# Performance work log

Measured on AMD Instinct MI355X. Metric: run time of the kernel, lower is better.

Reference implementation:

```python
import jax, jax.numpy as jnp
import numpy as np

N_ATOMS = 8000
N_PAIRS = 80000
NF_IN = 32
NF_OUT = 32
N_DIST = 16
N_COMP = 4      # l_max=1: [l=0 (1), l=1 (3)] tensor components
N_INV = 2       # _invariant_counts[(2, 1)]
MIND_SOFT = 0.85
MAXD_SOFT = 5.0
HARD_CUTOFF = 6.5
GN_EPS = 1e-5


def _sensitivity(dist, mu, sigma):
    # HIP-NN style inverse-distance Gaussians with smooth cos^2 cutoff.
    inv_d = 1.0 / dist                                   # (P,)
    base = jnp.exp(-0.5 * ((inv_d[:, None] - mu) / sigma) ** 2)  # (P, n_dist)
    cut = jnp.where(dist < HARD_CUTOFF,
                    jnp.cos(0.5 * jnp.pi * dist / HARD_CUTOFF) ** 2, 0.0)
    return base * cut[:, None]


def setup_inputs() -> dict:
    key = jax.random.key(0)
    ks = jax.random.split(key, 10)
    in_features = jax.random.normal(ks[0], (N_ATOMS, NF_IN), jnp.float32)
    pair_first = jnp.sort(jax.random.randint(ks[1], (N_PAIRS,), 0, N_ATOMS))
    pair_second = jax.random.randint(ks[2], (N_PAIRS,), 0, N_ATOMS)
    dist_pairs = (0.5 + (HARD_CUTOFF - 0.5)
                  * jax.random.uniform(ks[3], (N_PAIRS,), jnp.float32))
    tensor_rhats = jax.random.normal(ks[4], (N_PAIRS, N_COMP), jnp.float32)
    # learned params
    sens_mu = jnp.linspace(1.0 / MAXD_SOFT, 1.0 / MIND_SOFT, N_DIST).astype(jnp.float32)
    sens_sigma = jnp.full((N_DIST,), float(sens_mu[1] - sens_mu[0]), jnp.float32)
    s_int = (2.0 / (N_DIST * NF_IN + NF_OUT)) ** 0.5
    int_weights = s_int * jax.random.normal(ks[5], (N_DIST, NF_OUT, NF_IN), jnp.float32)
    s_self = (2.0 / (NF_IN + NF_OUT)) ** 0.5
    selfint_w = s_self * jax.random.normal(ks[6], (NF_OUT, NF_IN), jnp.float32)
    selfint_b = jnp.zeros((NF_OUT,), jnp.float32)
    s_mix = (2.0 / (N_INV * NF_OUT + NF_OUT)) ** 0.5
    mixing_weights = s_mix * jax.random.normal(ks[7], (NF_OUT, N_INV, NF_OUT), jnp.float32)
    gn_weight = jnp.ones((N_INV * NF_OUT,), jnp.float32)
    gn_bias = jnp.zeros((N_INV * NF_OUT,), jnp.float32)
    return {
        "in_features": in_features, "tensor_rhats": tensor_rhats,
        "dist_pairs": dist_pairs, "int_weights": int_weights,
        "selfint_w": selfint_w, "selfint_b": selfint_b,
        "mixing_weights": mixing_weights, "gn_weight": gn_weight,
        "gn_bias": gn_bias, "sens_mu": sens_mu, "sens_sigma": sens_sigma,
        "pair_first": pair_first, "pair_second": pair_second,
    }


def reference(in_features, tensor_rhats, dist_pairs, int_weights,
              selfint_w, selfint_b, mixing_weights, gn_weight, gn_bias,
              sens_mu, sens_sigma, pair_first, pair_second):
    n_atoms = in_features.shape[0]
    # self interaction (Linear)
    self_part = in_features @ selfint_w.T + selfint_b          # (N, nf_out)
    # tensor sensitivities: (P, n_comp, n_dist) -> flat (P, n_comp*n_dist)
    sense = _sensitivity(dist_pairs, sens_mu, sens_sigma)      # (P, n_dist)
    sense_flat = (tensor_rhats[:, :, None] * sense[:, None, :]).reshape(
        -1, N_COMP * N_DIST)
    # envsum: env[a, s, f] = sum_{p: pair_first[p]=a} sense_flat[p, s] * feat[pair_second[p], f]
    feat_j = in_features[pair_second]                          # (P, nf_in)
    contrib = sense_flat[:, :, None] * feat_j[:, None, :]      # (P, S, nf_in)
    env = jax.ops.segment_sum(contrib, pair_first, num_segments=n_atoms)
    # interaction weights contraction
    w_rs = jnp.transpose(int_weights, (0, 2, 1)).reshape(N_DIST * NF_IN, NF_OUT)
    env_rs = env.reshape(n_atoms * N_COMP, N_DIST * NF_IN)
    tf = (env_rs @ w_rs).reshape(n_atoms, N_COMP, NF_OUT)
    tf = jnp.transpose(tf, (0, 2, 1))                          # (N, nf_out, n_comp)
    # HopInvariantLayer (n_max=2, l_max=1): [l=0 scalar, |l=1 vector|^2]
    invariants = jnp.stack(
        [tf[..., 0], jnp.sum(tf[..., 1:] ** 2, axis=-1)], axis=-1)  # (N, nf_out, 2)
    # GroupNorm over channels (n_inv groups of nf_out channels)
    x = jnp.transpose(invariants, (0, 2, 1))                   # (N, n_inv, nf_out)
    mean = jnp.mean(x, axis=-1, keepdims=True)
    var = jnp.var(x, axis=-1, keepdims=True)
    xn = (x - mean) / jnp.sqrt(var + GN_EPS)
    xn = xn * gn_weight.reshape(N_INV, NF_OUT) + gn_bias.reshape(N_INV, NF_OUT)
    norm_inv = jnp.transpose(xn, (0, 2, 1)).reshape(n_atoms, NF_OUT * N_INV)
    mix = norm_inv @ mixing_weights.reshape(NF_OUT * N_INV, NF_OUT)
    return mix + self_part
```

## Files before the change

kernel.cpp:

```cpp
#include <hip/hip_runtime.h>
#include <hip/hip_bf16.h>
#include <stdint.h>

#define GN_EPS 1e-5f

typedef __fp16 half2_t __attribute__((ext_vector_type(2)));
typedef __fp16 v8h __attribute__((ext_vector_type(8)));
typedef float v4f __attribute__((ext_vector_type(4)));
union U32H2 { uint32_t u; half2_t h; };
union U4V8 { uint4 u; v8h h; };
union UF { uint32_t u; float f; };

__device__ __forceinline__ float ldin(const void* p, int i, bool bf) {
    if (bf) {
        UF c; c.u = ((uint32_t)((const uint16_t*)p)[i]) << 16;
        return c.f;
    }
    return ((const float*)p)[i];
}

__device__ __forceinline__ uint16_t f2bf(float x) {
    union { float f; uint32_t u; } c; c.f = x;
    uint32_t u = c.u;
    return (uint16_t)((u + 0x7FFFu + ((u >> 16) & 1u)) >> 16);
}

__device__ __forceinline__ bool detect_bf16(const void* gnw) {
    uint32_t det = *(const uint32_t*)gnw;
    return (det >> 16) == (det & 0xFFFFu);
}

__device__ __forceinline__ uint32_t pkh2(float lo, float hi) {
    U32H2 u; u.h = __builtin_amdgcn_cvt_pkrtz(lo, hi); return u.u;
}

__global__ __launch_bounds__(256) void k0_prep(
    const void* __restrict__ feat, const void* __restrict__ rhats,
    const void* __restrict__ dists, const void* __restrict__ intw,
    const void* __restrict__ selfw, const void* __restrict__ selfb,
    const void* __restrict__ mw, const void* __restrict__ gnw,
    const void* __restrict__ gnb, const void* __restrict__ mu,
    const void* __restrict__ sig, const int* __restrict__ pf,
    int* __restrict__ seg, uint32_t* __restrict__ Wmf,
    float* __restrict__ featf, float4* __restrict__ rc4,
    float2* __restrict__ dj2, const int* __restrict__ ps,
    float* __restrict__ mwf, uint32_t* __restrict__ selfh,
    float* __restrict__ gnwf, float* __restrict__ gnbf,
    float* __restrict__ selfbf, float* __restrict__ muf,
    float* __restrict__ isgf, int n_atoms, int n_pairs)
{
    const bool bf = detect_bf16(gnw);
    const int tid = blockIdx.x * 256 + threadIdx.x;

    if (tid < n_pairs) {
        int a0 = pf[tid];
        if (tid == 0) { for (int a = 0; a <= a0; ++a) seg[a] = 0; }
        if (tid + 1 < n_pairs) {
            int a1 = pf[tid + 1];
            for (int a = a0 + 1; a <= a1; ++a) seg[a] = tid + 1;
        } else {
            for (int a = a0 + 1; a <= n_atoms; ++a) seg[a] = n_pairs;
        }
        float dist = ldin(dists, tid, bf);
        float cd = __cosf(0.2416609733530613f * dist);
        float cut = (dist < 6.5f) ? cd * cd : 0.0f;
        float4 rc;
        rc.x = ldin(rhats, 4 * tid + 0, bf) * cut;
        rc.y = ldin(rhats, 4 * tid + 1, bf) * cut;
        rc.z = ldin(rhats, 4 * tid + 2, bf) * cut;
        rc.w = ldin(rhats, 4 * tid + 3, bf) * cut;
        rc4[tid] = rc;
        float2 dj; dj.x = 1.0f / dist; dj.y = __int_as_float(ps[tid]);
        dj2[tid] = dj;
    }
    {
        int i0 = tid * 4;
#pragma unroll
        for (int k = 0; k < 4; ++k) {
            int i = i0 + k;
            if (i < n_atoms * 32) featf[i] = ldin(feat, i, bf);
        }
    }
    if (tid < 8192) {
        int fp = tid & 15, d = (tid >> 4) & 15, o = tid >> 8;
        float wlo = ldin(intw, (d * 32 + o) * 32 + 2 * fp, bf);
        float whi = ldin(intw, (d * 32 + o) * 32 + 2 * fp + 1, bf);
        Wmf[tid] = pkh2(wlo, whi);
    }
    if (tid < 2048) mwf[tid] = ldin(mw, tid, bf);
    if (tid < 512) {
        int fp = tid & 15, o = tid >> 4;
        selfh[tid] = pkh2(ldin(selfw, o * 32 + 2 * fp, bf),
                          ldin(selfw, o * 32 + 2 * fp + 1, bf));
    }
    if (tid < 64) { gnwf[tid] = ldin(gnw, tid, bf); gnbf[tid] = ldin(gnb, tid, bf); }
    if (tid < 32) selfbf[tid] = ldin(selfb, tid, bf);
    if (tid < 16) { muf[tid] = ldin(mu, tid, bf); isgf[tid] = 1.0f / ldin(sig, tid, bf); }
}

__global__ __launch_bounds__(256, 4) void k2_main(
    const int* __restrict__ seg, const uint32_t* __restrict__ Wmf,
    const float* __restrict__ featf, const float4* __restrict__ rc4,
    const float2* __restrict__ dj2, const float* __restrict__ mwf,
    const uint32_t* __restrict__ selfh, const float* __restrict__ gnwf,
    const float* __restrict__ gnbf, const float* __restrict__ selfbf,
    const float* __restrict__ muf, const float* __restrict__ isgf,
    const void* __restrict__ gnw, void* __restrict__ out, int n_atoms)
{
    __shared__ uint32_t envs[16 * 256];
    __shared__ float tfs[4 * 32 * 4];
    __shared__ float selfs[4][32];
    __shared__ float mwTs[32 * 68];
    __shared__ float xns[4][64];

    const int t = threadIdx.x, wv = t >> 6, lane = t & 63;
    const int a0 = blockIdx.x * 4;
    int a = a0 + wv;
    const bool astore = (a < n_atoms);
    if (!astore) a = n_atoms - 1;

    {
        int o = t & 31, kc = t >> 5;
#pragma unroll
        for (int i = 0; i < 8; ++i) {
            int k = kc * 8 + i;
            mwTs[o * 68 + k] = mwf[k * 32 + o];
        }
    }

    const int dD = lane >> 2, fq = lane & 3;
    const float mu_d = muf[dD], isg_d = isgf[dD];

    float env[4][8];
#pragma unroll
    for (int c = 0; c < 4; ++c)
#pragma unroll
        for (int fl = 0; fl < 8; ++fl) env[c][fl] = 0.0f;

    const int s = seg[a], e = seg[a + 1];

    for (int p = s; p < e; p += 4) {
        float2 dj[4]; float4 rc[4];
#pragma unroll
        for (int i = 0; i < 4; ++i) {
            int pi = (p + i < e) ? p + i : e - 1;
            dj[i] = dj2[pi];
            float4 r = rc4[pi];
            if (p + i >= e) r = make_float4(0.f, 0.f, 0.f, 0.f);
            rc[i] = r;
        }
        float4 fa[4], fb[4];
#pragma unroll
        for (int i = 0; i < 4; ++i) {
            const float4* fr = (const float4*)(featf +
                (size_t)__float_as_int(dj[i].y) * 32) + fq * 2;
            fa[i] = fr[0]; fb[i] = fr[1];
        }
#pragma unroll
        for (int i = 0; i < 4; ++i) {
            float x = (dj[i].x - mu_d) * isg_d;
            float sd = __expf(-0.5f * x * x);
            float t0 = sd * rc[i].x, t1 = sd * rc[i].y;
            float t2 = sd * rc[i].z, t3 = sd * rc[i].w;
            float fj[8] = {fa[i].x, fa[i].y, fa[i].z, fa[i].w,
                           fb[i].x, fb[i].y, fb[i].z, fb[i].w};
#pragma unroll
            for (int fl = 0; fl < 8; ++fl) {
                env[0][fl] = fmaf(t0, fj[fl], env[0][fl]);
                env[1][fl] = fmaf(t1, fj[fl], env[1][fl]);
                env[2][fl] = fmaf(t2, fj[fl], env[2][fl]);
                env[3][fl] = fmaf(t3, fj[fl], env[3][fl]);
            }
        }
    }

    {
        const int ci = dD * 4 + fq;
#pragma unroll
        for (int c = 0; c < 4; ++c) {
            int m = wv * 4 + c;
            uint4 w;
            w.x = pkh2(env[c][0], env[c][1]);
            w.y = pkh2(env[c][2], env[c][3]);
            w.z = pkh2(env[c][4], env[c][5]);
            w.w = pkh2(env[c][6], env[c][7]);
            *(uint4*)&envs[m * 256 + ((ci ^ m) << 2)] = w;
        }
    }
    __syncthreads();

    const int mrow = lane & 15, quad = lane >> 4;
    const int tile = wv >> 1;
    const int og = tile * 16 + mrow;
    if ((wv & 1) == 0) {
        v4f acc = {0.f, 0.f, 0.f, 0.f};
        const uint4* wb = (const uint4*)Wmf + (og * 64 + quad);
#pragma unroll
        for (int kk = 0; kk < 16; ++kk) {
            int cia = kk * 4 + quad;
            U4V8 Af, Bf;
            Af.u = *(const uint4*)&envs[mrow * 256 + ((cia ^ mrow) << 2)];
            Bf.u = wb[kk * 4];
            acc = __builtin_amdgcn_mfma_f32_16x16x32_f16(Af.h, Bf.h, acc, 0, 0, 0);
        }
        float4 st; st.x = acc[0]; st.y = acc[1]; st.z = acc[2]; st.w = acc[3];
        *(float4*)&tfs[(quad * 32 + og) * 4] = st;
    } else {
        int ar = a0 + (mrow < 4 ? mrow : 0);
        if (ar >= n_atoms) ar = n_atoms - 1;
        const float4* fp4 = (const float4*)(featf + (size_t)ar * 32 + quad * 8);
        float4 x = fp4[0], y = fp4[1];
        U4V8 Af, Bf;
        Af.u = make_uint4(pkh2(x.x, x.y), pkh2(x.z, x.w),
                          pkh2(y.x, y.y), pkh2(y.z, y.w));
        Bf.u = *(const uint4*)(selfh + og * 16 + quad * 4);
        v4f acc = {0.f, 0.f, 0.f, 0.f};
        acc = __builtin_amdgcn_mfma_f32_16x16x32_f16(Af.h, Bf.h, acc, 0, 0, 0);
        if (quad == 0) {
#pragma unroll
            for (int r = 0; r < 4; ++r)
                selfs[r][og] = acc[r];
        }
    }
    __syncthreads();

    const int o = lane & 31, half = lane >> 5;
    float4 tf = *(const float4*)&tfs[(wv * 32 + o) * 4];
    float inv0 = tf.x;
    float inv1 = tf.y * tf.y + tf.z * tf.z + tf.w * tf.w;

    float s0 = inv0, q0 = inv0 * inv0, s1 = inv1, q1 = inv1 * inv1;
#pragma unroll
    for (int m = 16; m >= 1; m >>= 1) {
        s0 += __shfl_xor(s0, m, 32);
        q0 += __shfl_xor(q0, m, 32);
        s1 += __shfl_xor(s1, m, 32);
        q1 += __shfl_xor(q1, m, 32);
    }
    float mean0 = s0 * (1.f / 32.f), mean1 = s1 * (1.f / 32.f);
    float var0 = q0 * (1.f / 32.f) - mean0 * mean0;
    float var1 = q1 * (1.f / 32.f) - mean1 * mean1;
    float xn0 = (inv0 - mean0) * rsqrtf(var0 + GN_EPS);
    float xn1 = (inv1 - mean1) * rsqrtf(var1 + GN_EPS);
    xn0 = xn0 * gnwf[o] + gnbf[o];
    xn1 = xn1 * gnwf[32 + o] + gnbf[32 + o];

    if (half == 0) *(float2*)&xns[wv][2 * o] = make_float2(xn0, xn1);

    float mix = 0.0f;
#pragma unroll
    for (int c = 0; c < 16; ++c) {
        float4 xk = *(const float4*)&xns[wv][c * 4];
        float4 w4 = *(const float4*)&mwTs[o * 68 + c * 4];
        mix = fmaf(xk.x, w4.x, mix);
        mix = fmaf(xk.y, w4.y, mix);
        mix = fmaf(xk.z, w4.z, mix);
        mix = fmaf(xk.w, w4.w, mix);
    }

    float res = mix + selfs[wv][o] + selfbf[o];
    if (half == 0 && astore) {
        if (detect_bf16(gnw)) ((uint16_t*)out)[a * 32 + o] = f2bf(res);
        else                  ((float*)out)[a * 32 + o]    = res;
    }
}

extern "C" void kernel_launch(void* const* d_in, const int* in_sizes, int n_in,
                              void* d_out, int out_size, void* d_ws, size_t ws_size,
                              hipStream_t stream) {
    const void* feat  = d_in[0];
    const void* rhats = d_in[1];
    const void* dists = d_in[2];
    const void* intw  = d_in[3];
    const void* selfw = d_in[4];
    const void* selfb = d_in[5];
    const void* mw    = d_in[6];
    const void* gnw   = d_in[7];
    const void* gnb   = d_in[8];
    const void* mu    = d_in[9];
    const void* sig   = d_in[10];
    const int* pf     = (const int*)d_in[11];
    const int* ps     = (const int*)d_in[12];

    const int n_pairs = in_sizes[11];
    const int n_atoms = in_sizes[0] / 32;

    char* ws = (char*)d_ws;
    int*      seg    = (int*)(ws + 0);
    uint32_t* Wmf    = (uint32_t*)(ws + 32768);
    float*    featf  = (float*)(ws + 65536);
    float4*   rc4    = (float4*)(ws + 1089536);
    float2*   dj2    = (float2*)(ws + 2369536);
    float*    mwf    = (float*)(ws + 3009536);
    uint32_t* selfh  = (uint32_t*)(ws + 3017728);
    float*    gnwf   = (float*)(ws + 3021824);
    float*    gnbf   = (float*)(ws + 3022080);
    float*    selfbf = (float*)(ws + 3022336);
    float*    muf    = (float*)(ws + 3022464);
    float*    isgf   = (float*)(ws + 3022528);

    int thr = n_pairs;
    int feat_thr = (n_atoms * 32 + 3) / 4;
    if (feat_thr > thr) thr = feat_thr;
    if (thr < 8192) thr = 8192;
    hipLaunchKernelGGL(k0_prep, dim3((thr + 255) / 256), dim3(256), 0, stream,
                       feat, rhats, dists, intw, selfw, selfb, mw, gnw, gnb,
                       mu, sig, pf, seg, Wmf, featf, rc4, dj2, ps, mwf,
                       selfh, gnwf, gnbf, selfbf, muf, isgf, n_atoms, n_pairs);
    hipLaunchKernelGGL(k2_main, dim3((n_atoms + 3) / 4), dim3(256), 0, stream,
                       seg, Wmf, featf, rc4, dj2, mwf, selfh, gnwf, gnbf,
                       selfbf, muf, isgf, gnw, d_out, n_atoms);
}
```

Before: 110.4 us.

## Fuse prep kernel into main kernel and binary-search pair segments per atom

```diff
diff --git a/kernel.cpp b/kernel.cpp
--- a/kernel.cpp
+++ b/kernel.cpp
@@ -19,6 +19,9 @@
     return ((const float*)p)[i];
 }
 
+__device__ __forceinline__ float bfl(uint32_t u) { UF c; c.u = u << 16; return c.f; }
+__device__ __forceinline__ float bfh(uint32_t u) { UF c; c.u = u & 0xFFFF0000u; return c.f; }
+
 __device__ __forceinline__ uint16_t f2bf(float x) {
     union { float f; uint32_t u; } c; c.f = x;
     uint32_t u = c.u;
@@ -34,78 +37,15 @@
     U32H2 u; u.h = __builtin_amdgcn_cvt_pkrtz(lo, hi); return u.u;
 }
 
-__global__ __launch_bounds__(256) void k0_prep(
+__global__ __launch_bounds__(256, 4) void k_fused(
     const void* __restrict__ feat, const void* __restrict__ rhats,
     const void* __restrict__ dists, const void* __restrict__ intw,
     const void* __restrict__ selfw, const void* __restrict__ selfb,
     const void* __restrict__ mw, const void* __restrict__ gnw,
     const void* __restrict__ gnb, const void* __restrict__ mu,
     const void* __restrict__ sig, const int* __restrict__ pf,
-    int* __restrict__ seg, uint32_t* __restrict__ Wmf,
-    float* __restrict__ featf, float4* __restrict__ rc4,
-    float2* __restrict__ dj2, const int* __restrict__ ps,
-    float* __restrict__ mwf, uint32_t* __restrict__ selfh,
-    float* __restrict__ gnwf, float* __restrict__ gnbf,
-    float* __restrict__ selfbf, float* __restrict__ muf,
-    float* __restrict__ isgf, int n_atoms, int n_pairs)
-{
-    const bool bf = detect_bf16(gnw);
-    const int tid = blockIdx.x * 256 + threadIdx.x;
-
-    if (tid < n_pairs) {
-        int a0 = pf[tid];
-        if (tid == 0) { for (int a = 0; a <= a0; ++a) seg[a] = 0; }
-        if (tid + 1 < n_pairs) {
-            int a1 = pf[tid + 1];
-            for (int a = a0 + 1; a <= a1; ++a) seg[a] = tid + 1;
-        } else {
-            for (int a = a0 + 1; a <= n_atoms; ++a) seg[a] = n_pairs;
-        }
-        float dist = ldin(dists, tid, bf);
-        float cd = __cosf(0.2416609733530613f * dist);
-        float cut = (dist < 6.5f) ? cd * cd : 0.0f;
-        float4 rc;
-        rc.x = ldin(rhats, 4 * tid + 0, bf) * cut;
-        rc.y = ldin(rhats, 4 * tid + 1, bf) * cut;
-        rc.z = ldin(rhats, 4 * tid + 2, bf) * cut;
-        rc.w = ldin(rhats, 4 * tid + 3, bf) * cut;
-        rc4[tid] = rc;
-        float2 dj; dj.x = 1.0f / dist; dj.y = __int_as_float(ps[tid]);
-        dj2[tid] = dj;
-    }
-    {
-        int i0 = tid * 4;
-#pragma unroll
-        for (int k = 0; k < 4; ++k) {
-            int i = i0 + k;
-            if (i < n_atoms * 32) featf[i] = ldin(feat, i, bf);
-        }
-    }
-    if (tid < 8192) {
-        int fp = tid & 15, d = (tid >> 4) & 15, o = tid >> 8;
-        float wlo = ldin(intw, (d * 32 + o) * 32 + 2 * fp, bf);
-        float whi = ldin(intw, (d * 32 + o) * 32 + 2 * fp + 1, bf);
-        Wmf[tid] = pkh2(wlo, whi);
-    }
-    if (tid < 2048) mwf[tid] = ldin(mw, tid, bf);
-    if (tid < 512) {
-        int fp = tid & 15, o = tid >> 4;
-        selfh[tid] = pkh2(ldin(selfw, o * 32 + 2 * fp, bf),
-                          ldin(selfw, o * 32 + 2 * fp + 1, bf));
-    }
-    if (tid < 64) { gnwf[tid] = ldin(gnw, tid, bf); gnbf[tid] = ldin(gnb, tid, bf); }
-    if (tid < 32) selfbf[tid] = ldin(selfb, tid, bf);
-    if (tid < 16) { muf[tid] = ldin(mu, tid, bf); isgf[tid] = 1.0f / ldin(sig, tid, bf); }
-}
-
-__global__ __launch_bounds__(256, 4) void k2_main(
-    const int* __restrict__ seg, const uint32_t* __restrict__ Wmf,
-    const float* __restrict__ featf, const float4* __restrict__ rc4,
-    const float2* __restrict__ dj2, const float* __restrict__ mwf,
-    const uint32_t* __restrict__ selfh, const float* __restrict__ gnwf,
-    const float* __restrict__ gnbf, const float* __restrict__ selfbf,
-    const float* __restrict__ muf, const float* __restrict__ isgf,
-    const void* __restrict__ gnw, void* __restrict__ out, int n_atoms)
+    const int* __restrict__ ps, void* __restrict__ out,
+    int n_atoms, int n_pairs)
 {
     __shared__ uint32_t envs[16 * 256];
     __shared__ float tfs[4 * 32 * 4];
@@ -114,6 +54,7 @@
     __shared__ float xns[4][64];
 
     const int t = threadIdx.x, wv = t >> 6, lane = t & 63;
+    const bool bf = detect_bf16(gnw);
     const int a0 = blockIdx.x * 4;
     int a = a0 + wv;
     const bool astore = (a < n_atoms);
@@ -124,12 +65,24 @@
 #pragma unroll
         for (int i = 0; i < 8; ++i) {
             int k = kc * 8 + i;
-            mwTs[o * 68 + k] = mwf[k * 32 + o];
+            mwTs[o * 68 + k] = ldin(mw, k * 32 + o, bf);
         }
     }
 
     const int dD = lane >> 2, fq = lane & 3;
-    const float mu_d = muf[dD], isg_d = isgf[dD];
+    const float mu_d = ldin(mu, dD, bf);
+    const float isg_d = 1.0f / ldin(sig, dD, bf);
+
+    int lo0 = 0, hi0 = n_pairs, lo1 = 0, hi1 = n_pairs;
+    while (lo0 < hi0 || lo1 < hi1) {
+        bool c0 = lo0 < hi0, c1 = lo1 < hi1;
+        int m0 = (lo0 + hi0) >> 1, m1 = (lo1 + hi1) >> 1;
+        int v0 = pf[c0 ? m0 : 0];
+        int v1 = pf[c1 ? m1 : 0];
+        if (c0) { if (v0 < a) lo0 = m0 + 1; else hi0 = m0; }
+        if (c1) { if (v1 < a + 1) lo1 = m1 + 1; else hi1 = m1; }
+    }
+    const int s = lo0, e = hi1;
 
     float env[4][8];
 #pragma unroll
@@ -137,39 +90,70 @@
 #pragma unroll
         for (int fl = 0; fl < 8; ++fl) env[c][fl] = 0.0f;
 
-    const int s = seg[a], e = seg[a + 1];
-
     for (int p = s; p < e; p += 4) {
-        float2 dj[4]; float4 rc[4];
+        int pi[4], jv[4];
+#pragma unroll
+        for (int i = 0; i < 4; ++i) pi[i] = (p + i < e) ? p + i : e - 1;
+#pragma unroll
+        for (int i = 0; i < 4; ++i) jv[i] = ps[pi[i]];
+
+        float dv[4]; float4 rh[4];
+        if (bf) {
+#pragma unroll
+            for (int i = 0; i < 4; ++i) {
+                dv[i] = bfl((uint32_t)((const uint16_t*)dists)[pi[i]]);
+                const uint32_t* rp = (const uint32_t*)rhats + 2 * pi[i];
+                uint32_t r0 = rp[0], r1 = rp[1];
+                rh[i] = make_float4(bfl(r0), bfh(r0), bfl(r1), bfh(r1));
+            }
+        } else {
+#pragma unroll
+            for (int i = 0; i < 4; ++i) {
+                dv[i] = ((const float*)dists)[pi[i]];
+                rh[i] = *(const float4*)((const float*)rhats + 4 * pi[i]);
+            }
+        }
+
+        float fj[4][8];
+        if (bf) {
+#pragma unroll
+            for (int i = 0; i < 4; ++i) {
+                uint4 v = *(const uint4*)((const uint16_t*)feat +
+                                          (size_t)jv[i] * 32 + fq * 8);
+                fj[i][0] = bfl(v.x); fj[i][1] = bfh(v.x);
+                fj[i][2] = bfl(v.y); fj[i][3] = bfh(v.y);
+                fj[i][4] = bfl(v.z); fj[i][5] = bfh(v.z);
+                fj[i][6] = bfl(v.w); fj[i][7] = bfh(v.w);
+            }
+        } else {
+#pragma unroll
+            for (int i = 0; i < 4; ++i) {
+                const float4* fr = (const float4*)((const float*)feat +
+                                                   (size_t)jv[i] * 32) + fq * 2;
+                float4 fa = fr[0], fb = fr[1];
+                fj[i][0] = fa.x; fj[i][1] = fa.y; fj[i][2] = fa.z; fj[i][3] = fa.w;
+                fj[i][4] = fb.x; fj[i][5] = fb.y; fj[i][6] = fb.z; fj[i][7] = fb.w;
+            }
+        }
+
 #pragma unroll
         for (int i = 0; i < 4; ++i) {
-            int pi = (p + i < e) ? p + i : e - 1;
-            dj[i] = dj2[pi];
-            float4 r = rc4[pi];
-            if (p + i >= e) r = make_float4(0.f, 0.f, 0.f, 0.f);
-            rc[i] = r;
-        }
-        float4 fa[4], fb[4];
-#pragma unroll
-        for (int i = 0; i < 4; ++i) {
-            const float4* fr = (const float4*)(featf +
-                (size_t)__float_as_int(dj[i].y) * 32) + fq * 2;
-            fa[i] = fr[0]; fb[i] = fr[1];
-        }
-#pragma unroll
-        for (int i = 0; i < 4; ++i) {
-            float x = (dj[i].x - mu_d) * isg_d;
+            float dist = dv[i];
+            float cd = __cosf(0.2416609733530613f * dist);
+            float cut = (dist < 6.5f) ? cd * cd : 0.0f;
+            if (p + i >= e) cut = 0.0f;
+            float rcx = rh[i].x * cut, rcy = rh[i].y * cut;
+            float rcz = rh[i].z * cut, rcw = rh[i].w * cut;
+            float inv = 1.0f / dist;
+            float x = (inv - mu_d) * isg_d;
             float sd = __expf(-0.5f * x * x);
-            float t0 = sd * rc[i].x, t1 = sd * rc[i].y;
-            float t2 = sd * rc[i].z, t3 = sd * rc[i].w;
-            float fj[8] = {fa[i].x, fa[i].y, fa[i].z, fa[i].w,
-                           fb[i].x, fb[i].y, fb[i].z, fb[i].w};
+            float t0 = sd * rcx, t1 = sd * rcy, t2 = sd * rcz, t3 = sd * rcw;
 #pragma unroll
             for (int fl = 0; fl < 8; ++fl) {
-                env[0][fl] = fmaf(t0, fj[fl], env[0][fl]);
-                env[1][fl] = fmaf(t1, fj[fl], env[1][fl]);
-                env[2][fl] = fmaf(t2, fj[fl], env[2][fl]);
-                env[3][fl] = fmaf(t3, fj[fl], env[3][fl]);
+                env[0][fl] = fmaf(t0, fj[i][fl], env[0][fl]);
+                env[1][fl] = fmaf(t1, fj[i][fl], env[1][fl]);
+                env[2][fl] = fmaf(t2, fj[i][fl], env[2][fl]);
+                env[3][fl] = fmaf(t3, fj[i][fl], env[3][fl]);
             }
         }
     }
@@ -190,30 +174,59 @@
     __syncthreads();
 
     const int mrow = lane & 15, quad = lane >> 4;
-    const int tile = wv >> 1;
-    const int og = tile * 16 + mrow;
+    const int og = (wv >> 1) * 16 + mrow;
     if ((wv & 1) == 0) {
         v4f acc = {0.f, 0.f, 0.f, 0.f};
-        const uint4* wb = (const uint4*)Wmf + (og * 64 + quad);
-#pragma unroll
-        for (int kk = 0; kk < 16; ++kk) {
-            int cia = kk * 4 + quad;
-            U4V8 Af, Bf;
-            Af.u = *(const uint4*)&envs[mrow * 256 + ((cia ^ mrow) << 2)];
-            Bf.u = wb[kk * 4];
-            acc = __builtin_amdgcn_mfma_f32_16x16x32_f16(Af.h, Bf.h, acc, 0, 0, 0);
+        if (bf) {
+#pragma unroll 4
+            for (int kk = 0; kk < 16; ++kk) {
+                const uint16_t* wp = (const uint16_t*)intw +
+                    ((size_t)(kk * 32 + og)) * 32 + quad * 8;
+                uint4 v = *(const uint4*)wp;
+                U4V8 Af, Bf;
+                Bf.u = make_uint4(pkh2(bfl(v.x), bfh(v.x)), pkh2(bfl(v.y), bfh(v.y)),
+                                  pkh2(bfl(v.z), bfh(v.z)), pkh2(bfl(v.w), bfh(v.w)));
+                int cia = kk * 4 + quad;
+                Af.u = *(const uint4*)&envs[mrow * 256 + ((cia ^ mrow) << 2)];
+                acc = __builtin_amdgcn_mfma_f32_16x16x32_f16(Af.h, Bf.h, acc, 0, 0, 0);
+            }
+        } else {
+#pragma unroll 4
+            for (int kk = 0; kk < 16; ++kk) {
+                const float* wp = (const float*)intw +
+                    ((size_t)(kk * 32 + og)) * 32 + quad * 8;
+                float4 w0 = *(const float4*)wp, w1 = *(const float4*)(wp + 4);
+                U4V8 Af, Bf;
+                Bf.u = make_uint4(pkh2(w0.x, w0.y), pkh2(w0.z, w0.w),
+                                  pkh2(w1.x, w1.y), pkh2(w1.z, w1.w));
+                int cia = kk * 4 + quad;
+                Af.u = *(const uint4*)&envs[mrow * 256 + ((cia ^ mrow) << 2)];
+                acc = __builtin_amdgcn_mfma_f32_16x16x32_f16(Af.h, Bf.h, acc, 0, 0, 0);
+            }
         }
         float4 st; st.x = acc[0]; st.y = acc[1]; st.z = acc[2]; st.w = acc[3];
         *(float4*)&tfs[(quad * 32 + og) * 4] = st;
     } else {
         int ar = a0 + (mrow < 4 ? mrow : 0);
         if (ar >= n_atoms) ar = n_atoms - 1;
-        const float4* fp4 = (const float4*)(featf + (size_t)ar * 32 + quad * 8);
-        float4 x = fp4[0], y = fp4[1];
         U4V8 Af, Bf;
-        Af.u = make_uint4(pkh2(x.x, x.y), pkh2(x.z, x.w),
-                          pkh2(y.x, y.y), pkh2(y.z, y.w));
-        Bf.u = *(const uint4*)(selfh + og * 16 + quad * 4);
+        if (bf) {
+            uint4 v = *(const uint4*)((const uint16_t*)feat + (size_t)ar * 32 + quad * 8);
+            Af.u = make_uint4(pkh2(bfl(v.x), bfh(v.x)), pkh2(bfl(v.y), bfh(v.y)),
+                              pkh2(bfl(v.z), bfh(v.z)), pkh2(bfl(v.w), bfh(v.w)));
+            uint4 w = *(const uint4*)((const uint16_t*)selfw + (size_t)og * 32 + quad * 8);
+            Bf.u = make_uint4(pkh2(bfl(w.x), bfh(w.x)), pkh2(bfl(w.y), bfh(w.y)),
+                              pkh2(bfl(w.z), bfh(w.z)), pkh2(bfl(w.w), bfh(w.w)));
+        } else {
+            const float* fp = (const float*)feat + (size_t)ar * 32 + quad * 8;
+            float4 x = *(const float4*)fp, y = *(const float4*)(fp + 4);
+            Af.u = make_uint4(pkh2(x.x, x.y), pkh2(x.z, x.w),
+                              pkh2(y.x, y.y), pkh2(y.z, y.w));
+            const float* sp = (const float*)selfw + (size_t)og * 32 + quad * 8;
+            float4 s0 = *(const float4*)sp, s1 = *(const float4*)(sp + 4);
+            Bf.u = make_uint4(pkh2(s0.x, s0.y), pkh2(s0.z, s0.w),
+                              pkh2(s1.x, s1.y), pkh2(s1.z, s1.w));
+        }
         v4f acc = {0.f, 0.f, 0.f, 0.f};
         acc = __builtin_amdgcn_mfma_f32_16x16x32_f16(Af.h, Bf.h, acc, 0, 0, 0);
         if (quad == 0) {
@@ -242,8 +255,8 @@
     float var1 = q1 * (1.f / 32.f) - mean1 * mean1;
     float xn0 = (inv0 - mean0) * rsqrtf(var0 + GN_EPS);
     float xn1 = (inv1 - mean1) * rsqrtf(var1 + GN_EPS);
-    xn0 = xn0 * gnwf[o] + gnbf[o];
-    xn1 = xn1 * gnwf[32 + o] + gnbf[32 + o];
+    xn0 = xn0 * ldin(gnw, o, bf) + ldin(gnb, o, bf);
+    xn1 = xn1 * ldin(gnw, 32 + o, bf) + ldin(gnb, 32 + o, bf);
 
     if (half == 0) *(float2*)&xns[wv][2 * o] = make_float2(xn0, xn1);
 
@@ -258,10 +271,10 @@
         mix = fmaf(xk.w, w4.w, mix);
     }
 
-    float res = mix + selfs[wv][o] + selfbf[o];
+    float res = mix + selfs[wv][o] + ldin(selfb, o, bf);
     if (half == 0 && astore) {
-        if (detect_bf16(gnw)) ((uint16_t*)out)[a * 32 + o] = f2bf(res);
-        else                  ((float*)out)[a * 32 + o]    = res;
+        if (bf) ((uint16_t*)out)[a * 32 + o] = f2bf(res);
+        else    ((float*)out)[a * 32 + o]    = res;
     }
 }
 
@@ -285,29 +298,8 @@
     const int n_pairs = in_sizes[11];
     const int n_atoms = in_sizes[0] / 32;
 
-    char* ws = (char*)d_ws;
-    int*      seg    = (int*)(ws + 0);
-    uint32_t* Wmf    = (uint32_t*)(ws + 32768);
-    float*    featf  = (float*)(ws + 65536);
-    float4*   rc4    = (float4*)(ws + 1089536);
-    float2*   dj2    = (float2*)(ws + 2369536);
-    float*    mwf    = (float*)(ws + 3009536);
-    uint32_t* selfh  = (uint32_t*)(ws + 3017728);
-    float*    gnwf   = (float*)(ws + 3021824);
-    float*    gnbf   = (float*)(ws + 3022080);
-    float*    selfbf = (float*)(ws + 3022336);
-    float*    muf    = (float*)(ws + 3022464);
-    float*    isgf   = (float*)(ws + 3022528);
-
-    int thr = n_pairs;
-    int feat_thr = (n_atoms * 32 + 3) / 4;
-    if (feat_thr > thr) thr = feat_thr;
-    if (thr < 8192) thr = 8192;
-    hipLaunchKernelGGL(k0_prep, dim3((thr + 255) / 256), dim3(256), 0, stream,
+    (void)d_ws; (void)ws_size;
+    hipLaunchKernelGGL(k_fused, dim3((n_atoms + 3) / 4), dim3(256), 0, stream,
                        feat, rhats, dists, intw, selfw, selfb, mw, gnw, gnb,
-                       mu, sig, pf, seg, Wmf, featf, rc4, dj2, ps, mwf,
-                       selfh, gnwf, gnbf, selfbf, muf, isgf, n_atoms, n_pairs);
-    hipLaunchKernelGGL(k2_main, dim3((n_atoms + 3) / 4), dim3(256), 0, stream,
-                       seg, Wmf, featf, rc4, dj2, mwf, selfh, gnwf, gnbf,
-                       selfbf, muf, isgf, gnw, d_out, n_atoms);
-}
+                       mu, sig, pf, ps, d_out, n_atoms, n_pairs);
+}
```

Result: slower. 126.0 us (+14.1%).
